# Optimization experiments

Measured on AMD Instinct MI355X. Metric: run time of the kernel, lower is better.

Reference implementation:

```python
import jax, jax.numpy as jnp
import numpy as np

B, N, RIN, ROUT, DEMB, FIN, FE, E, ITERS = 64, 128, 32, 64, 64, 64, 16, 65536, 3
NTOT = B * N


def gnn(x, edge_index, edge_feat, Ws, Wm, We, b):
    # edge-conditioned message passing: [NTOT, Fin] -> [NTOT, Fout]
    src, dst = edge_index[0], edge_index[1]
    msg = jax.nn.relu(x[src] @ Wm + edge_feat @ We)          # [E, Fout]
    agg = jax.ops.segment_sum(msg, dst, num_segments=x.shape[0])
    return jax.nn.relu(x @ Ws + agg + b)


def setup_inputs() -> dict:
    key = jax.random.key(0)
    ks = jax.random.split(key, 20)
    s = 0.1
    return {
        "x_r": jax.random.normal(ks[0], (NTOT, FIN), jnp.float32),
        "edge_index_r": jax.random.randint(ks[1], (2, E), 0, NTOT),
        "edge_feat_r": jax.random.normal(ks[2], (E, FE), jnp.float32),
        "x_p": jax.random.normal(ks[3], (NTOT, FIN), jnp.float32),
        "edge_index_p": jax.random.randint(ks[4], (2, E), 0, NTOT),
        "edge_feat_p": jax.random.normal(ks[5], (E, FE), jnp.float32),
        "r_mask": jnp.ones((B, N), dtype=bool),
        "p_mask": jnp.ones((B, N), dtype=bool),
        # gnn_1 params (FIN -> DEMB)
        "g1_Ws": jax.random.normal(ks[6], (FIN, DEMB)) * s,
        "g1_Wm": jax.random.normal(ks[7], (FIN, DEMB)) * s,
        "g1_We": jax.random.normal(ks[8], (FE, DEMB)) * s,
        "g1_b": jnp.zeros((DEMB,), jnp.float32),
        # gnn_2 params (RIN -> ROUT)
        "g2_Ws": jax.random.normal(ks[9], (RIN, ROUT)) * s,
        "g2_Wm": jax.random.normal(ks[10], (RIN, ROUT)) * s,
        "g2_We": jax.random.normal(ks[11], (FE, ROUT)) * s,
        "g2_b": jnp.zeros((ROUT,), jnp.float32),
        # consensus mlp (ROUT -> ROUT -> 1)
        "mlp_W1": jax.random.normal(ks[12], (ROUT, ROUT)) * s,
        "mlp_b1": jnp.zeros((ROUT,), jnp.float32),
        "mlp_W2": jax.random.normal(ks[13], (ROUT, 1)) * s,
        "mlp_b2": jnp.zeros((1,), jnp.float32),
    }


def reference(x_r, edge_index_r, edge_feat_r, x_p, edge_index_p, edge_feat_p,
              r_mask, p_mask,
              g1_Ws, g1_Wm, g1_We, g1_b,
              g2_Ws, g2_Wm, g2_We, g2_b,
              mlp_W1, mlp_b1, mlp_W2, mlp_b2):
    # node embeddings via gnn_1, then dense-batch to [B, N, DEMB]
    h_r = gnn(x_r, edge_index_r, edge_feat_r, g1_Ws, g1_Wm, g1_We, g1_b).reshape(B, N, DEMB)
    h_p = gnn(x_p, edge_index_p, edge_feat_p, g1_Ws, g1_Wm, g1_We, g1_b).reshape(B, N, DEMB)

    M_hat = jnp.einsum('brd,bpd->brp', h_r, h_p)             # [B, N_r, N_p]
    M_mask = r_mask[:, :, None] & p_mask[:, None, :]
    M_0 = jax.nn.softmax(M_hat, axis=-1).reshape(NTOT, N)    # packed (full mask)

    rkey = jax.random.key(42)
    for it in range(ITERS):
        M = jax.nn.softmax(M_hat, axis=-1)
        rf_r = jax.random.normal(jax.random.fold_in(rkey, it), (B, N, RIN), jnp.float32)
        rf_p = jnp.einsum('brp,bri->bpi', M, rf_r)           # M^T @ rand
        o_r = gnn(rf_r.reshape(NTOT, RIN), edge_index_r, edge_feat_r,
                  g2_Ws, g2_Wm, g2_We, g2_b).reshape(B, N, ROUT)
        o_p = gnn(rf_p.reshape(NTOT, RIN), edge_index_p, edge_feat_p,
                  g2_Ws, g2_Wm, g2_We, g2_b).reshape(B, N, ROUT)
        D = o_r[:, :, None, :] - o_p[:, None, :, :]          # [B, N_r, N_p, ROUT]
        upd = (jax.nn.relu(D @ mlp_W1 + mlp_b1) @ mlp_W2 + mlp_b2)[..., 0]
        M_hat = M_hat + jnp.where(M_mask, upd, 0.0)

    M_T = jax.nn.softmax(M_hat, axis=-1).reshape(NTOT, N)
    return (M_0, M_T)
```

## Files before the change

### kernel.cpp

```cpp
#include <hip/hip_runtime.h>

constexpr int kE = 65536, kNTOT = 8192;

__host__ __device__ __forceinline__ void tf_round(unsigned& x0, unsigned& x1, int r) {
  x0 += x1;
  x1 = (x1 << r) | (x1 >> (32 - r));
  x1 ^= x0;
}
__host__ __device__ __forceinline__ void tf2x32(unsigned k0, unsigned k1,
                                                unsigned& x0, unsigned& x1) {
  unsigned ks2 = k0 ^ k1 ^ 0x1BD11BDAu;
  x0 += k0; x1 += k1;
  tf_round(x0,x1,13); tf_round(x0,x1,15); tf_round(x0,x1,26); tf_round(x0,x1,6);
  x0 += k1; x1 += ks2 + 1u;
  tf_round(x0,x1,17); tf_round(x0,x1,29); tf_round(x0,x1,16); tf_round(x0,x1,24);
  x0 += ks2; x1 += k0 + 2u;
  tf_round(x0,x1,13); tf_round(x0,x1,15); tf_round(x0,x1,26); tf_round(x0,x1,6);
  x0 += k0; x1 += k1 + 3u;
  tf_round(x0,x1,17); tf_round(x0,x1,29); tf_round(x0,x1,16); tf_round(x0,x1,24);
  x0 += k1; x1 += ks2 + 4u;
  tf_round(x0,x1,13); tf_round(x0,x1,15); tf_round(x0,x1,26); tf_round(x0,x1,6);
  x0 += ks2; x1 += k0 + 5u;
}

__device__ __forceinline__ float bits_to_normal(unsigned bits) {
  float f = __uint_as_float((bits >> 9) | 0x3f800000u) - 1.0f;
  const float LO = -0.99999994f;
  float u = fmaf(f, 2.0f, LO);
  u = fmaxf(u, LO);
  float w = -log1pf(-u * u);
  float p;
  if (w < 5.0f) {
    w -= 2.5f;
    p = 2.81022636e-08f;
    p = fmaf(p, w, 3.43273939e-07f);
    p = fmaf(p, w, -3.5233877e-06f);
    p = fmaf(p, w, -4.39150654e-06f);
    p = fmaf(p, w, 0.00021858087f);
    p = fmaf(p, w, -0.00125372503f);
    p = fmaf(p, w, -0.00417768164f);
    p = fmaf(p, w, 0.246640727f);
    p = fmaf(p, w, 1.50140941f);
  } else {
    w = sqrtf(w) - 3.0f;
    p = -0.000200214257f;
    p = fmaf(p, w, 0.000100950558f);
    p = fmaf(p, w, 0.00134934322f);
    p = fmaf(p, w, -0.00367342844f);
    p = fmaf(p, w, 0.00573950773f);
    p = fmaf(p, w, -0.0076224613f);
    p = fmaf(p, w, 0.00943887047f);
    p = fmaf(p, w, 1.00167406f);
    p = fmaf(p, w, 2.83297682f);
  }
  return 1.41421356f * (p * u);
}

__device__ __forceinline__ float redmax32(float v) {
#pragma unroll
  for (int o = 16; o > 0; o >>= 1) v = fmaxf(v, __shfl_xor(v, o));
  return v;
}
__device__ __forceinline__ float redsum32(float v) {
#pragma unroll
  for (int o = 16; o > 0; o >>= 1) v += __shfl_xor(v, o);
  return v;
}

__global__ __launch_bounds__(256) void hist_kern(const int* __restrict__ eiR,
                                                 const int* __restrict__ eiP,
                                                 int* __restrict__ offR,
                                                 int* __restrict__ offP,
                                                 float* __restrict__ aggz,
                                                 float* __restrict__ rfpz) {
  int i = blockIdx.x * 256 + threadIdx.x;
  float4 z4 = make_float4(0.f, 0.f, 0.f, 0.f);
  float4* z = reinterpret_cast<float4*>(aggz) + i * 2;
  z[0] = z4; z[1] = z4;
  reinterpret_cast<float2*>(rfpz)[i] = make_float2(0.f, 0.f);
  const int* ei = (i < kE) ? eiR : eiP;
  int* off = (i < kE) ? offR : offP;
  int e = i & (kE - 1);
  atomicAdd(&off[ei[kE + e]], 1);
}

__global__ __launch_bounds__(256) void scan_kern(int* __restrict__ offR,
                                                 int* __restrict__ offP) {
  int* off = blockIdx.x ? offP : offR;
  int t = threadIdx.x;
  int base = t * 32;
  int v[32];
#pragma unroll
  for (int i = 0; i < 32; ++i) v[i] = off[base + i];
  int sum = 0;
#pragma unroll
  for (int i = 0; i < 32; ++i) sum += v[i];
  int lane = t & 63, w = t >> 6;
  int incl = sum;
#pragma unroll
  for (int o = 1; o < 64; o <<= 1) {
    int y = __shfl_up(incl, o);
    if (lane >= o) incl += y;
  }
  __shared__ int wsum[4];
  if (lane == 63) wsum[w] = incl;
  __syncthreads();
  int woff = 0;
#pragma unroll
  for (int i = 0; i < 4; ++i) if (i < w) woff += wsum[i];
  int running = woff + incl - sum;
#pragma unroll
  for (int i = 0; i < 32; ++i) {
    off[base + i] = running;
    running += v[i];
  }
}

__global__ __launch_bounds__(256) void scatter_kern(
    const int* __restrict__ eiR, const int* __restrict__ eiP,
    int* __restrict__ offR, int* __restrict__ offP,
    int* __restrict__ permR, int* __restrict__ permP,
    int* __restrict__ srcsR, int* __restrict__ srcsP,
    int* __restrict__ dstsR, int* __restrict__ dstsP) {
  int i = blockIdx.x * 256 + threadIdx.x;
  const int* ei = (i < kE) ? eiR : eiP;
  int* off = (i < kE) ? offR : offP;
  int* perm = (i < kE) ? permR : permP;
  int* srcs = (i < kE) ? srcsR : srcsP;
  int* dsts = (i < kE) ? dstsR : dstsP;
  int e = i & (kE - 1);
  int dst = ei[kE + e];
  int pos = atomicAdd(&off[dst], 1);
  perm[pos] = e;
  srcs[pos] = ei[e];
  dsts[pos] = dst;
}

template <int KK>
__global__ __launch_bounds__(256) void xw_gemm(
    const float* __restrict__ inR, const float* __restrict__ inP,
    float* __restrict__ xwR, float* __restrict__ xwP,
    const float* __restrict__ W) {
  __shared__ float sX[KK][68];
  __shared__ float sW[KK][68];
  bool isP = blockIdx.x >= 128;
  const float* in = isP ? inP : inR;
  float* xw = isP ? xwP : xwR;
  int n0 = (blockIdx.x & 127) * 64;
  int t = threadIdx.x;
#pragma unroll
  for (int idx = 0; idx < KK * 64 / 1024; ++idx) {
    int q = t * 4 + idx * 1024;
    int k = q >> 6, j = q & 63;
    *reinterpret_cast<float4*>(&sW[k][j]) = *reinterpret_cast<const float4*>(W + q);
    int r = q / KK, kk = q & (KK - 1);
    float4 v = *reinterpret_cast<const float4*>(in + (size_t)n0 * KK + q);
    sX[kk][r] = v.x; sX[kk + 1][r] = v.y; sX[kk + 2][r] = v.z; sX[kk + 3][r] = v.w;
  }
  __syncthreads();
  int tn = (t & 15) * 4, tj = (t >> 4) * 4;
  float acc[4][4] = {};
#pragma unroll 8
  for (int k = 0; k < KK; ++k) {
    float4 a = *reinterpret_cast<const float4*>(&sX[k][tn]);
    float4 b = *reinterpret_cast<const float4*>(&sW[k][tj]);
    acc[0][0] = fmaf(a.x, b.x, acc[0][0]); acc[0][1] = fmaf(a.x, b.y, acc[0][1]);
    acc[0][2] = fmaf(a.x, b.z, acc[0][2]); acc[0][3] = fmaf(a.x, b.w, acc[0][3]);
    acc[1][0] = fmaf(a.y, b.x, acc[1][0]); acc[1][1] = fmaf(a.y, b.y, acc[1][1]);
    acc[1][2] = fmaf(a.y, b.z, acc[1][2]); acc[1][3] = fmaf(a.y, b.w, acc[1][3]);
    acc[2][0] = fmaf(a.z, b.x, acc[2][0]); acc[2][1] = fmaf(a.z, b.y, acc[2][1]);
    acc[2][2] = fmaf(a.z, b.z, acc[2][2]); acc[2][3] = fmaf(a.z, b.w, acc[2][3]);
    acc[3][0] = fmaf(a.w, b.x, acc[3][0]); acc[3][1] = fmaf(a.w, b.y, acc[3][1]);
    acc[3][2] = fmaf(a.w, b.z, acc[3][2]); acc[3][3] = fmaf(a.w, b.w, acc[3][3]);
  }
#pragma unroll
  for (int i = 0; i < 4; ++i) {
    *reinterpret_cast<float4*>(&xw[(size_t)(n0 + tn + i) * 64 + tj]) =
        make_float4(acc[i][0], acc[i][1], acc[i][2], acc[i][3]);
  }
}

__global__ __launch_bounds__(256) void msg_edge(
    const float* __restrict__ xwR, const float* __restrict__ efR,
    const int* __restrict__ srcsR, const int* __restrict__ permR,
    const int* __restrict__ dstsR, float* __restrict__ aggR,
    const float* __restrict__ xwP, const float* __restrict__ efP,
    const int* __restrict__ srcsP, const int* __restrict__ permP,
    const int* __restrict__ dstsP, float* __restrict__ aggP,
    const float* __restrict__ We) {
  __shared__ float sEF[16][68];
  __shared__ float sW[16][68];
  __shared__ float sOut[64][68];
  __shared__ int sDst[64];
  __shared__ int sSrc[64];
  __shared__ int sPerm[64];
  bool isP = blockIdx.x >= 1024;
  const float* xw = isP ? xwP : xwR;
  const float* ef = isP ? efP : efR;
  const int* srcs = isP ? srcsP : srcsR;
  const int* perm = isP ? permP : permR;
  const int* dsts = isP ? dstsP : dstsR;
  float* agg = isP ? aggP : aggR;
  int i0 = (blockIdx.x & 1023) * 64;
  int t = threadIdx.x;
  {
    int q = t * 4;
    int k = q >> 6, j = q & 63;
    *reinterpret_cast<float4*>(&sW[k][j]) = *reinterpret_cast<const float4*>(We + q);
  }
  if (t < 64) {
    sDst[t] = dsts[i0 + t];
    sSrc[t] = srcs[i0 + t];
    sPerm[t] = perm[i0 + t];
  }
  __syncthreads();
  {
    int l = t & 3;
    int g = t >> 2;
    int rb = g >> 2;
    int kq = g & 3;
    int gbase = (t & 63) & ~3;
    int k4 = kq * 4;
    int r = rb * 4 + l;
    const float* rptr = ef + (size_t)sPerm[r] * 16 + k4;
    float4 v = *reinterpret_cast<const float4*>(rptr);
    float vc[4] = {v.x, v.y, v.z, v.w};
    float out[4];
#pragma unroll
    for (int c = 0; c < 4; ++c) {
      float val = vc[(l - c) & 3];
      out[(l + c) & 3] = __shfl(val, gbase + ((l + c) & 3), 64);
    }
    *reinterpret_cast<float4*>(&sEF[k4 + l][rb * 4]) =
        make_float4(out[0], out[1], out[2], out[3]);
  }
  __syncthreads();
  int tn = (t & 15) * 4, tj = (t >> 4) * 4;
  float acc[4][4] = {};
#pragma unroll
  for (int k = 0; k < 16; ++k) {
    float4 a = *reinterpret_cast<const float4*>(&sEF[k][tn]);
    float4 b = *reinterpret_cast<const float4*>(&sW[k][tj]);
    acc[0][0] = fmaf(a.x, b.x, acc[0][0]); acc[0][1] = fmaf(a.x, b.y, acc[0][1]);
    acc[0][2] = fmaf(a.x, b.z, acc[0][2]); acc[0][3] = fmaf(a.x, b.w, acc[0][3]);
    acc[1][0] = fmaf(a.y, b.x, acc[1][0]); acc[1][1] = fmaf(a.y, b.y, acc[1][1]);
    acc[1][2] = fmaf(a.y, b.z, acc[1][2]); acc[1][3] = fmaf(a.y, b.w, acc[1][3]);
    acc[2][0] = fmaf(a.z, b.x, acc[2][0]); acc[2][1] = fmaf(a.z, b.y, acc[2][1]);
    acc[2][2] = fmaf(a.z, b.z, acc[2][2]); acc[2][3] = fmaf(a.z, b.w, acc[2][3]);
    acc[3][0] = fmaf(a.w, b.x, acc[3][0]); acc[3][1] = fmaf(a.w, b.y, acc[3][1]);
    acc[3][2] = fmaf(a.w, b.z, acc[3][2]); acc[3][3] = fmaf(a.w, b.w, acc[3][3]);
  }
#pragma unroll
  for (int i = 0; i < 4; ++i) {
    float4 g = *reinterpret_cast<const float4*>(xw + (size_t)sSrc[tn + i] * 64 + tj);
    *reinterpret_cast<float4*>(&sOut[tn + i][tj]) =
        make_float4(fmaxf(acc[i][0] + g.x, 0.f), fmaxf(acc[i][1] + g.y, 0.f),
                    fmaxf(acc[i][2] + g.z, 0.f), fmaxf(acc[i][3] + g.w, 0.f));
  }
  __syncthreads();
  int col = t & 63;
  int r0l = (t >> 6) * 16;
  float run = 0.f;
  int rd = sDst[r0l];
#pragma unroll
  for (int r = 0; r < 16; ++r) {
    int d = sDst[r0l + r];
    if (d != rd) {
      unsafeAtomicAdd(&agg[(size_t)rd * 64 + col], run);
      run = 0.f; rd = d;
    }
    run += sOut[r0l + r][col];
  }
  unsafeAtomicAdd(&agg[(size_t)rd * 64 + col], run);
}

__global__ __launch_bounds__(256) void node1_gemm(
    const float* __restrict__ xR, float* __restrict__ aggR, float* __restrict__ hR,
    const float* __restrict__ xP, float* __restrict__ aggP, float* __restrict__ hP,
    const float* __restrict__ Ws, const float* __restrict__ bias) {
  __shared__ float sX[64][68];
  __shared__ float sW[64][68];
  bool isP = blockIdx.x >= 128;
  const float* x = isP ? xP : xR;
  float* agg = isP ? aggP : aggR;
  float* h = isP ? hP : hR;
  int n0 = (blockIdx.x & 127) * 64;
  int t = threadIdx.x;
#pragma unroll
  for (int idx = 0; idx < 4; ++idx) {
    int q = t * 4 + idx * 1024;
    int k = q >> 6, j = q & 63;
    *reinterpret_cast<float4*>(&sW[k][j]) = *reinterpret_cast<const float4*>(Ws + q);
    float4 v = *reinterpret_cast<const float4*>(x + (size_t)n0 * 64 + q);
    sX[j + 0][k] = v.x; sX[j + 1][k] = v.y; sX[j + 2][k] = v.z; sX[j + 3][k] = v.w;
  }
  __syncthreads();
  int tn = (t & 15) * 4, tj = (t >> 4) * 4;
  float acc[4][4] = {};
#pragma unroll 8
  for (int k = 0; k < 64; ++k) {
    float4 a = *reinterpret_cast<const float4*>(&sX[k][tn]);
    float4 b = *reinterpret_cast<const float4*>(&sW[k][tj]);
    acc[0][0] = fmaf(a.x, b.x, acc[0][0]); acc[0][1] = fmaf(a.x, b.y, acc[0][1]);
    acc[0][2] = fmaf(a.x, b.z, acc[0][2]); acc[0][3] = fmaf(a.x, b.w, acc[0][3]);
    acc[1][0] = fmaf(a.y, b.x, acc[1][0]); acc[1][1] = fmaf(a.y, b.y, acc[1][1]);
    acc[1][2] = fmaf(a.y, b.z, acc[1][2]); acc[1][3] = fmaf(a.y, b.w, acc[1][3]);
    acc[2][0] = fmaf(a.z, b.x, acc[2][0]); acc[2][1] = fmaf(a.z, b.y, acc[2][1]);
    acc[2][2] = fmaf(a.z, b.z, acc[2][2]); acc[2][3] = fmaf(a.z, b.w, acc[2][3]);
    acc[3][0] = fmaf(a.w, b.x, acc[3][0]); acc[3][1] = fmaf(a.w, b.y, acc[3][1]);
    acc[3][2] = fmaf(a.w, b.z, acc[3][2]); acc[3][3] = fmaf(a.w, b.w, acc[3][3]);
  }
  float4 bv = *reinterpret_cast<const float4*>(bias + tj);
  float4 z4 = make_float4(0.f, 0.f, 0.f, 0.f);
#pragma unroll
  for (int i = 0; i < 4; ++i) {
    int n = n0 + tn + i;
    float4 g = *reinterpret_cast<const float4*>(&agg[(size_t)n * 64 + tj]);
    *reinterpret_cast<float4*>(&agg[(size_t)n * 64 + tj]) = z4;
    float4 o;
    o.x = fmaxf(acc[i][0] + g.x + bv.x, 0.f);
    o.y = fmaxf(acc[i][1] + g.y + bv.y, 0.f);
    o.z = fmaxf(acc[i][2] + g.z + bv.z, 0.f);
    o.w = fmaxf(acc[i][3] + g.w + bv.w, 0.f);
    *reinterpret_cast<float4*>(&h[(size_t)n * 64 + tj]) = o;
  }
}

__device__ __forceinline__ void rfp_partial(const float sm[16][128],
                                            const float rfb[16][32],
                                            float* __restrict__ rfpB, int t) {
  float rfc[16];
  int iw = t & 31;
#pragma unroll
  for (int r = 0; r < 16; ++r) rfc[r] = rfb[r][iw];
#pragma unroll
  for (int rep = 0; rep < 16; ++rep) {
    int p = rep * 8 + (t >> 5);
    float a = 0.f;
#pragma unroll
    for (int r = 0; r < 16; ++r) a = fmaf(sm[r][p], rfc[r], a);
    unsafeAtomicAdd(&rfpB[p * 32 + iw], a);
  }
}

__device__ __forceinline__ void gen_rfr_tile(float* __restrict__ rfr,
                                             float rfb[16][32], int b, int r0,
                                             int t, unsigned fk0, unsigned fk1) {
  unsigned base = (unsigned)((b * 128 + r0) * 32);
#pragma unroll
  for (int q = 0; q < 2; ++q) {
    unsigned j = (unsigned)(q * 256 + t);
    unsigned i = base + j;
    unsigned a0 = 0u, a1 = i;
    tf2x32(fk0, fk1, a0, a1);
    float v = bits_to_normal(a0 ^ a1);
    rfr[i] = v;
    rfb[j >> 5][j & 31] = v;
  }
}

__global__ __launch_bounds__(256) void mhat_soft(
    const float* __restrict__ hR, const float* __restrict__ hP,
    float* __restrict__ Mhat, float* __restrict__ M0out,
    float* __restrict__ rfr, float* __restrict__ rfp,
    unsigned fk0, unsigned fk1) {
  __shared__ float hr[16][66];
  __shared__ float hp[128][66];
  __shared__ float sm[16][128];
  __shared__ float rfb[16][32];
  int gid = blockIdx.x, t = threadIdx.x;
  int b = gid >> 3, r0 = (gid & 7) * 16;
  gen_rfr_tile(rfr, rfb, b, r0, t, fk0, fk1);
  const float* hrG = hR + ((size_t)(b * 128 + r0)) * 64;
  {
    int q = t * 4; int r = q >> 6, d = q & 63;
    float4 v = *reinterpret_cast<const float4*>(hrG + q);
    hr[r][d] = v.x; hr[r][d + 1] = v.y; hr[r][d + 2] = v.z; hr[r][d + 3] = v.w;
  }
  const float* hpG = hP + (size_t)b * 128 * 64;
#pragma unroll
  for (int rep = 0; rep < 8; ++rep) {
    int q = (rep * 256 + t) * 4; int p = q >> 6, d = q & 63;
    float4 v = *reinterpret_cast<const float4*>(hpG + q);
    hp[p][d] = v.x; hp[p][d + 1] = v.y; hp[p][d + 2] = v.z; hp[p][d + 3] = v.w;
  }
  __syncthreads();
  int tx = t & 31, ty = t >> 5;
  float acc[2][4] = {};
  for (int d = 0; d < 64; ++d) {
    float a0 = hr[ty][d], a1 = hr[ty + 8][d];
    float q0 = hp[tx][d], q1 = hp[tx + 32][d], q2 = hp[tx + 64][d], q3 = hp[tx + 96][d];
    acc[0][0] = fmaf(a0, q0, acc[0][0]); acc[0][1] = fmaf(a0, q1, acc[0][1]);
    acc[0][2] = fmaf(a0, q2, acc[0][2]); acc[0][3] = fmaf(a0, q3, acc[0][3]);
    acc[1][0] = fmaf(a1, q0, acc[1][0]); acc[1][1] = fmaf(a1, q1, acc[1][1]);
    acc[1][2] = fmaf(a1, q2, acc[1][2]); acc[1][3] = fmaf(a1, q3, acc[1][3]);
  }
#pragma unroll
  for (int ii = 0; ii < 2; ++ii) {
    int r = r0 + ty + 8 * ii;
    float* mrow = Mhat + ((size_t)(b * 128 + r)) * 128;
    mrow[tx] = acc[ii][0]; mrow[tx + 32] = acc[ii][1];
    mrow[tx + 64] = acc[ii][2]; mrow[tx + 96] = acc[ii][3];
    float mx = redmax32(fmaxf(fmaxf(acc[ii][0], acc[ii][1]), fmaxf(acc[ii][2], acc[ii][3])));
    float e0 = __expf(acc[ii][0] - mx), e1 = __expf(acc[ii][1] - mx);
    float e2 = __expf(acc[ii][2] - mx), e3 = __expf(acc[ii][3] - mx);
    float inv = 1.0f / redsum32(e0 + e1 + e2 + e3);
    float* orow = M0out + ((size_t)(b * 128 + r)) * 128;
    orow[tx] = e0 * inv; orow[tx + 32] = e1 * inv;
    orow[tx + 64] = e2 * inv; orow[tx + 96] = e3 * inv;
    int rl = ty + 8 * ii;
    sm[rl][tx] = e0 * inv; sm[rl][tx + 32] = e1 * inv;
    sm[rl][tx + 64] = e2 * inv; sm[rl][tx + 96] = e3 * inv;
  }
  __syncthreads();
  rfp_partial(sm, rfb, rfp + (size_t)b * 4096, t);
}

__global__ __launch_bounds__(256) void node2u_gemm(
    const float* __restrict__ rfR, float* __restrict__ aggR, float* __restrict__ uR,
    const float* __restrict__ rfP, float* __restrict__ aggP, float* __restrict__ uP,
    const float* __restrict__ Ws2, const float* __restrict__ g2b,
    const float* __restrict__ W1, const float* __restrict__ b1,
    float* __restrict__ rfp_clear) {
  __shared__ float sRF[32][68];
  __shared__ float sW2[32][68];
  __shared__ float sW1[64][68];
  __shared__ float sO[64][68];
  bool isP = blockIdx.x >= 128;
  const float* rf = isP ? rfP : rfR;
  float* agg = isP ? aggP : aggR;
  float* u = isP ? uP : uR;
  int n0 = (blockIdx.x & 127) * 64;
  int t = threadIdx.x;
#pragma unroll
  for (int idx = 0; idx < 4; ++idx) {
    int q = t * 4 + idx * 1024;
    *reinterpret_cast<float4*>(&sW1[q >> 6][q & 63]) = *reinterpret_cast<const float4*>(W1 + q);
  }
#pragma unroll
  for (int idx = 0; idx < 2; ++idx) {
    int q = t * 4 + idx * 1024;
    *reinterpret_cast<float4*>(&sW2[q >> 6][q & 63]) = *reinterpret_cast<const float4*>(Ws2 + q);
    int r = q >> 5, kk = q & 31;
    float4 v = *reinterpret_cast<const float4*>(rf + (size_t)(n0 + r) * 32 + kk);
    sRF[kk][r] = v.x; sRF[kk + 1][r] = v.y; sRF[kk + 2][r] = v.z; sRF[kk + 3][r] = v.w;
  }
  __syncthreads();
  if (isP) {
    float4 z4 = make_float4(0.f, 0.f, 0.f, 0.f);
    float4* rz = reinterpret_cast<float4*>(rfp_clear + (size_t)n0 * 32);
    rz[t * 2] = z4; rz[t * 2 + 1] = z4;
  }
  int tn = (t & 15) * 4, tj = (t >> 4) * 4;
  float acc[4][4] = {};
#pragma unroll 8
  for (int k = 0; k < 32; ++k) {
    float4 a = *reinterpret_cast<const float4*>(&sRF[k][tn]);
    float4 b = *reinterpret_cast<const float4*>(&sW2[k][tj]);
    acc[0][0] = fmaf(a.x, b.x, acc[0][0]); acc[0][1] = fmaf(a.x, b.y, acc[0][1]);
    acc[0][2] = fmaf(a.x, b.z, acc[0][2]); acc[0][3] = fmaf(a.x, b.w, acc[0][3]);
    acc[1][0] = fmaf(a.y, b.x, acc[1][0]); acc[1][1] = fmaf(a.y, b.y, acc[1][1]);
    acc[1][2] = fmaf(a.y, b.z, acc[1][2]); acc[1][3] = fmaf(a.y, b.w, acc[1][3]);
    acc[2][0] = fmaf(a.z, b.x, acc[2][0]); acc[2][1] = fmaf(a.z, b.y, acc[2][1]);
    acc[2][2] = fmaf(a.z, b.z, acc[2][2]); acc[2][3] = fmaf(a.z, b.w, acc[2][3]);
    acc[3][0] = fmaf(a.w, b.x, acc[3][0]); acc[3][1] = fmaf(a.w, b.y, acc[3][1]);
    acc[3][2] = fmaf(a.w, b.z, acc[3][2]); acc[3][3] = fmaf(a.w, b.w, acc[3][3]);
  }
  float4 bg = *reinterpret_cast<const float4*>(g2b + tj);
  float4 z4 = make_float4(0.f, 0.f, 0.f, 0.f);
#pragma unroll
  for (int i = 0; i < 4; ++i) {
    int n = n0 + tn + i;
    float4 g = *reinterpret_cast<const float4*>(&agg[(size_t)n * 64 + tj]);
    *reinterpret_cast<float4*>(&agg[(size_t)n * 64 + tj]) = z4;
    sO[tj + 0][tn + i] = fmaxf(acc[i][0] + g.x + bg.x, 0.f);
    sO[tj + 1][tn + i] = fmaxf(acc[i][1] + g.y + bg.y, 0.f);
    sO[tj + 2][tn + i] = fmaxf(acc[i][2] + g.z + bg.z, 0.f);
    sO[tj + 3][tn + i] = fmaxf(acc[i][3] + g.w + bg.w, 0.f);
  }
  __syncthreads();
  float acc2[4][4] = {};
#pragma unroll 8
  for (int k = 0; k < 64; ++k) {
    float4 a = *reinterpret_cast<const float4*>(&sO[k][tn]);
    float4 b = *reinterpret_cast<const float4*>(&sW1[k][tj]);
    acc2[0][0] = fmaf(a.x, b.x, acc2[0][0]); acc2[0][1] = fmaf(a.x, b.y, acc2[0][1]);
    acc2[0][2] = fmaf(a.x, b.z, acc2[0][2]); acc2[0][3] = fmaf(a.x, b.w, acc2[0][3]);
    acc2[1][0] = fmaf(a.y, b.x, acc2[1][0]); acc2[1][1] = fmaf(a.y, b.y, acc2[1][1]);
    acc2[1][2] = fmaf(a.y, b.z, acc2[1][2]); acc2[1][3] = fmaf(a.y, b.w, acc2[1][3]);
    acc2[2][0] = fmaf(a.z, b.x, acc2[2][0]); acc2[2][1] = fmaf(a.z, b.y, acc2[2][1]);
    acc2[2][2] = fmaf(a.z, b.z, acc2[2][2]); acc2[2][3] = fmaf(a.z, b.w, acc2[2][3]);
    acc2[3][0] = fmaf(a.w, b.x, acc2[3][0]); acc2[3][1] = fmaf(a.w, b.y, acc2[3][1]);
    acc2[3][2] = fmaf(a.w, b.z, acc2[3][2]); acc2[3][3] = fmaf(a.w, b.w, acc2[3][3]);
  }
  float4 b1v = make_float4(0.f, 0.f, 0.f, 0.f);
  if (!isP) b1v = *reinterpret_cast<const float4*>(b1 + tj);
#pragma unroll
  for (int i = 0; i < 4; ++i) {
    int n = n0 + tn + i;
    float4 o;
    o.x = acc2[i][0] + b1v.x; o.y = acc2[i][1] + b1v.y;
    o.z = acc2[i][2] + b1v.z; o.w = acc2[i][3] + b1v.w;
    *reinterpret_cast<float4*>(&u[(size_t)n * 64 + tj]) = o;
  }
}

__global__ __launch_bounds__(256) void upd_soft(
    const float* __restrict__ uR, const float* __restrict__ uP,
    const float* __restrict__ W2, const float* __restrict__ b2p,
    float* __restrict__ Mhat, float* __restrict__ outLast, int last,
    float* __restrict__ rfr, float* __restrict__ rfp,
    unsigned fk0, unsigned fk1) {
  __shared__ float sur[16][66];
  __shared__ float sup[128][66];
  __shared__ float sw2[64];
  __shared__ float sm[16][128];
  __shared__ float rfb[16][32];
  int gid = blockIdx.x, t = threadIdx.x;
  int b = gid >> 3, r0 = (gid & 7) * 16;
  if (!last) gen_rfr_tile(rfr, rfb, b, r0, t, fk0, fk1);
  const float* urG = uR + ((size_t)(b * 128 + r0)) * 64;
  {
    int q = t * 4; int r = q >> 6, d = q & 63;
    float4 v = *reinterpret_cast<const float4*>(urG + q);
    sur[r][d] = v.x; sur[r][d + 1] = v.y; sur[r][d + 2] = v.z; sur[r][d + 3] = v.w;
  }
  const float* upG = uP + (size_t)b * 128 * 64;
#pragma unroll
  for (int rep = 0; rep < 8; ++rep) {
    int q = (rep * 256 + t) * 4; int p = q >> 6, d = q & 63;
    float4 v = *reinterpret_cast<const float4*>(upG + q);
    sup[p][d] = v.x; sup[p][d + 1] = v.y; sup[p][d + 2] = v.z; sup[p][d + 3] = v.w;
  }
  if (t < 64) sw2[t] = W2[t];
  __syncthreads();
  int tx = t & 31, ty = t >> 5;
  float acc[2][4] = {};
  for (int j = 0; j < 64; ++j) {
    float w2v = sw2[j];
    float a0 = sur[ty][j], a1 = sur[ty + 8][j];
    float q0 = sup[tx][j], q1 = sup[tx + 32][j], q2 = sup[tx + 64][j], q3 = sup[tx + 96][j];
    acc[0][0] = fmaf(fmaxf(a0 - q0, 0.f), w2v, acc[0][0]);
    acc[0][1] = fmaf(fmaxf(a0 - q1, 0.f), w2v, acc[0][1]);
    acc[0][2] = fmaf(fmaxf(a0 - q2, 0.f), w2v, acc[0][2]);
    acc[0][3] = fmaf(fmaxf(a0 - q3, 0.f), w2v, acc[0][3]);
    acc[1][0] = fmaf(fmaxf(a1 - q0, 0.f), w2v, acc[1][0]);
    acc[1][1] = fmaf(fmaxf(a1 - q1, 0.f), w2v, acc[1][1]);
    acc[1][2] = fmaf(fmaxf(a1 - q2, 0.f), w2v, acc[1][2]);
    acc[1][3] = fmaf(fmaxf(a1 - q3, 0.f), w2v, acc[1][3]);
  }
  float b2v = b2p[0];
#pragma unroll
  for (int ii = 0; ii < 2; ++ii) {
    int r = r0 + ty + 8 * ii;
    float* mrow = Mhat + ((size_t)(b * 128 + r)) * 128;
    float m0 = mrow[tx] + acc[ii][0] + b2v;
    float m1 = mrow[tx + 32] + acc[ii][1] + b2v;
    float m2 = mrow[tx + 64] + acc[ii][2] + b2v;
    float m3 = mrow[tx + 96] + acc[ii][3] + b2v;
    if (!last) {
      mrow[tx] = m0; mrow[tx + 32] = m1; mrow[tx + 64] = m2; mrow[tx + 96] = m3;
    }
    float mx = redmax32(fmaxf(fmaxf(m0, m1), fmaxf(m2, m3)));
    float e0 = __expf(m0 - mx), e1 = __expf(m1 - mx);
    float e2 = __expf(m2 - mx), e3 = __expf(m3 - mx);
    float inv = 1.0f / redsum32(e0 + e1 + e2 + e3);
    if (last) {
      float* orow = outLast + ((size_t)(b * 128 + r)) * 128;
      orow[tx] = e0 * inv; orow[tx + 32] = e1 * inv;
      orow[tx + 64] = e2 * inv; orow[tx + 96] = e3 * inv;
    } else {
      int rl = ty + 8 * ii;
      sm[rl][tx] = e0 * inv; sm[rl][tx + 32] = e1 * inv;
      sm[rl][tx + 64] = e2 * inv; sm[rl][tx + 96] = e3 * inv;
    }
  }
  if (!last) {
    __syncthreads();
    rfp_partial(sm, rfb, rfp + (size_t)b * 4096, t);
  }
}

extern "C" void kernel_launch(void* const* d_in, const int* in_sizes, int n_in,
                              void* d_out, int out_size, void* d_ws, size_t ws_size,
                              hipStream_t stream) {
  (void)in_sizes; (void)n_in; (void)out_size; (void)ws_size;
  const float* x_r  = (const float*)d_in[0];
  const int*   ei_r = (const int*)d_in[1];
  const float* ef_r = (const float*)d_in[2];
  const float* x_p  = (const float*)d_in[3];
  const int*   ei_p = (const int*)d_in[4];
  const float* ef_p = (const float*)d_in[5];
  const float* g1_Ws = (const float*)d_in[8];
  const float* g1_Wm = (const float*)d_in[9];
  const float* g1_We = (const float*)d_in[10];
  const float* g1_b  = (const float*)d_in[11];
  const float* g2_Ws = (const float*)d_in[12];
  const float* g2_Wm = (const float*)d_in[13];
  const float* g2_We = (const float*)d_in[14];
  const float* g2_b  = (const float*)d_in[15];
  const float* W1 = (const float*)d_in[16];
  const float* b1 = (const float*)d_in[17];
  const float* W2 = (const float*)d_in[18];
  const float* b2 = (const float*)d_in[19];
  float* out = (float*)d_out;

  float* ws = (float*)d_ws;
  float* h_r   = ws;
  float* h_p   = h_r + 524288;
  float* Mhat  = h_p + 524288;
  float* rfr   = Mhat + 1048576;
  float* rfp   = rfr + 262144;
  float* u_r   = rfp + 262144;
  float* u_p   = u_r + 524288;
  float* agg_r = u_p + 524288;
  float* agg_p = agg_r + 524288;
  float* xw_r  = agg_p + 524288;
  float* xw_p  = xw_r + 524288;
  int* ib      = (int*)(xw_p + 524288);
  int* off_r  = ib;
  int* off_p  = off_r + 8192;
  int* perm_r = off_p + 8192;
  int* perm_p = perm_r + 65536;
  int* srcs_r = perm_p + 65536;
  int* srcs_p = srcs_r + 65536;
  int* dsts_r = srcs_p + 65536;
  int* dsts_p = dsts_r + 65536;

  unsigned fk0[3], fk1[3];
  for (int it = 0; it < 3; ++it) {
    unsigned a = 0u, c = (unsigned)it;
    tf2x32(0u, 42u, a, c);
    fk0[it] = a; fk1[it] = c;
  }

  hipMemsetAsync(off_r, 0, 2 * 8192 * sizeof(int), stream);
  hist_kern<<<512, 256, 0, stream>>>(ei_r, ei_p, off_r, off_p, agg_r, rfp);
  scan_kern<<<2, 256, 0, stream>>>(off_r, off_p);
  scatter_kern<<<512, 256, 0, stream>>>(ei_r, ei_p, off_r, off_p,
                                        perm_r, perm_p, srcs_r, srcs_p,
                                        dsts_r, dsts_p);

  xw_gemm<64><<<256, 256, 0, stream>>>(x_r, x_p, xw_r, xw_p, g1_Wm);
  msg_edge<<<2048, 256, 0, stream>>>(xw_r, ef_r, srcs_r, perm_r, dsts_r, agg_r,
                                     xw_p, ef_p, srcs_p, perm_p, dsts_p, agg_p,
                                     g1_We);
  node1_gemm<<<256, 256, 0, stream>>>(x_r, agg_r, h_r, x_p, agg_p, h_p, g1_Ws, g1_b);
  mhat_soft<<<512, 256, 0, stream>>>(h_r, h_p, Mhat, out, rfr, rfp, fk0[0], fk1[0]);

  for (int it = 0; it < 3; ++it) {
    xw_gemm<32><<<256, 256, 0, stream>>>(rfr, rfp, xw_r, xw_p, g2_Wm);
    msg_edge<<<2048, 256, 0, stream>>>(xw_r, ef_r, srcs_r, perm_r, dsts_r, agg_r,
                                       xw_p, ef_p, srcs_p, perm_p, dsts_p, agg_p,
                                       g2_We);
    node2u_gemm<<<256, 256, 0, stream>>>(rfr, agg_r, u_r, rfp, agg_p, u_p,
                                         g2_Ws, g2_b, W1, b1, rfp);
    int last = (it == 2);
    upd_soft<<<512, 256, 0, stream>>>(u_r, u_p, W2, b2, Mhat,
                                      out + 1048576, last,
                                      rfr, rfp,
                                      fk0[it < 2 ? it + 1 : 0], fk1[it < 2 ? it + 1 : 0]);
  }
}
```

Baseline: 284.2 us.

## Precompute loop-invariant edge-feature projection and fuse rf_r projection into softmax kernels

The edge_feat @ g2_We product does not change across iterations, so it is now computed once inside the first message kernel and stored per edge (two 16 MB buffers). The per-iteration message kernel then only gathers that stored projection plus the source projection, with no edge-feature GEMM and no permuted edge-feature loads. The rf_r @ Wm projection is computed inside the kernels that generate rf_r, which leaves a smaller GEMM for rf_p only. The cost is extra workspace and global-memory traffic for reading 64-wide per-edge projections in place of 16-wide edge features, plus more shared memory in the softmax kernels.

Measured after the change: 289.8 us. Within noise of the previous version (+2.0%).

```diff
diff --git a/kernel.cpp b/kernel.cpp
--- a/kernel.cpp
+++ b/kernel.cpp
@@ -180,16 +180,55 @@
   }
 }
 
-__global__ __launch_bounds__(256) void msg_edge(
+__global__ __launch_bounds__(256) void xwp_gemm(
+    const float* __restrict__ rfp, float* __restrict__ xwP,
+    const float* __restrict__ W) {
+  __shared__ float sX[32][68];
+  __shared__ float sW[32][68];
+  int n0 = blockIdx.x * 64;
+  int t = threadIdx.x;
+#pragma unroll
+  for (int idx = 0; idx < 2; ++idx) {
+    int q = t * 4 + idx * 1024;
+    *reinterpret_cast<float4*>(&sW[q >> 6][q & 63]) = *reinterpret_cast<const float4*>(W + q);
+    int r = q >> 5, kk = q & 31;
+    float4 v = *reinterpret_cast<const float4*>(rfp + (size_t)n0 * 32 + q);
+    sX[kk][r] = v.x; sX[kk + 1][r] = v.y; sX[kk + 2][r] = v.z; sX[kk + 3][r] = v.w;
+  }
+  __syncthreads();
+  int tn = (t & 15) * 4, tj = (t >> 4) * 4;
+  float acc[4][4] = {};
+#pragma unroll 8
+  for (int k = 0; k < 32; ++k) {
+    float4 a = *reinterpret_cast<const float4*>(&sX[k][tn]);
+    float4 b = *reinterpret_cast<const float4*>(&sW[k][tj]);
+    acc[0][0] = fmaf(a.x, b.x, acc[0][0]); acc[0][1] = fmaf(a.x, b.y, acc[0][1]);
+    acc[0][2] = fmaf(a.x, b.z, acc[0][2]); acc[0][3] = fmaf(a.x, b.w, acc[0][3]);
+    acc[1][0] = fmaf(a.y, b.x, acc[1][0]); acc[1][1] = fmaf(a.y, b.y, acc[1][1]);
+    acc[1][2] = fmaf(a.y, b.z, acc[1][2]); acc[1][3] = fmaf(a.y, b.w, acc[1][3]);
+    acc[2][0] = fmaf(a.z, b.x, acc[2][0]); acc[2][1] = fmaf(a.z, b.y, acc[2][1]);
+    acc[2][2] = fmaf(a.z, b.z, acc[2][2]); acc[2][3] = fmaf(a.z, b.w, acc[2][3]);
+    acc[3][0] = fmaf(a.w, b.x, acc[3][0]); acc[3][1] = fmaf(a.w, b.y, acc[3][1]);
+    acc[3][2] = fmaf(a.w, b.z, acc[3][2]); acc[3][3] = fmaf(a.w, b.w, acc[3][3]);
+  }
+#pragma unroll
+  for (int i = 0; i < 4; ++i) {
+    *reinterpret_cast<float4*>(&xwP[(size_t)(n0 + tn + i) * 64 + tj]) =
+        make_float4(acc[i][0], acc[i][1], acc[i][2], acc[i][3]);
+  }
+}
+
+__global__ __launch_bounds__(256) void msg_edge_g1(
     const float* __restrict__ xwR, const float* __restrict__ efR,
     const int* __restrict__ srcsR, const int* __restrict__ permR,
-    const int* __restrict__ dstsR, float* __restrict__ aggR,
+    const int* __restrict__ dstsR, float* __restrict__ aggR, float* __restrict__ ew2R,
     const float* __restrict__ xwP, const float* __restrict__ efP,
     const int* __restrict__ srcsP, const int* __restrict__ permP,
-    const int* __restrict__ dstsP, float* __restrict__ aggP,
-    const float* __restrict__ We) {
+    const int* __restrict__ dstsP, float* __restrict__ aggP, float* __restrict__ ew2P,
+    const float* __restrict__ We1, const float* __restrict__ We2) {
   __shared__ float sEF[16][68];
-  __shared__ float sW[16][68];
+  __shared__ float sW1[16][68];
+  __shared__ float sW2[16][68];
   __shared__ float sOut[64][68];
   __shared__ int sDst[64];
   __shared__ int sSrc[64];
@@ -201,12 +240,14 @@
   const int* perm = isP ? permP : permR;
   const int* dsts = isP ? dstsP : dstsR;
   float* agg = isP ? aggP : aggR;
+  float* ew2 = isP ? ew2P : ew2R;
   int i0 = (blockIdx.x & 1023) * 64;
   int t = threadIdx.x;
   {
     int q = t * 4;
     int k = q >> 6, j = q & 63;
-    *reinterpret_cast<float4*>(&sW[k][j]) = *reinterpret_cast<const float4*>(We + q);
+    *reinterpret_cast<float4*>(&sW1[k][j]) = *reinterpret_cast<const float4*>(We1 + q);
+    *reinterpret_cast<float4*>(&sW2[k][j]) = *reinterpret_cast<const float4*>(We2 + q);
   }
   if (t < 64) {
     sDst[t] = dsts[i0 + t];
@@ -237,10 +278,12 @@
   __syncthreads();
   int tn = (t & 15) * 4, tj = (t >> 4) * 4;
   float acc[4][4] = {};
+  float ac2[4][4] = {};
 #pragma unroll
   for (int k = 0; k < 16; ++k) {
     float4 a = *reinterpret_cast<const float4*>(&sEF[k][tn]);
-    float4 b = *reinterpret_cast<const float4*>(&sW[k][tj]);
+    float4 b = *reinterpret_cast<const float4*>(&sW1[k][tj]);
+    float4 c = *reinterpret_cast<const float4*>(&sW2[k][tj]);
     acc[0][0] = fmaf(a.x, b.x, acc[0][0]); acc[0][1] = fmaf(a.x, b.y, acc[0][1]);
     acc[0][2] = fmaf(a.x, b.z, acc[0][2]); acc[0][3] = fmaf(a.x, b.w, acc[0][3]);
     acc[1][0] = fmaf(a.y, b.x, acc[1][0]); acc[1][1] = fmaf(a.y, b.y, acc[1][1]);
@@ -249,13 +292,72 @@
     acc[2][2] = fmaf(a.z, b.z, acc[2][2]); acc[2][3] = fmaf(a.z, b.w, acc[2][3]);
     acc[3][0] = fmaf(a.w, b.x, acc[3][0]); acc[3][1] = fmaf(a.w, b.y, acc[3][1]);
     acc[3][2] = fmaf(a.w, b.z, acc[3][2]); acc[3][3] = fmaf(a.w, b.w, acc[3][3]);
+    ac2[0][0] = fmaf(a.x, c.x, ac2[0][0]); ac2[0][1] = fmaf(a.x, c.y, ac2[0][1]);
+    ac2[0][2] = fmaf(a.x, c.z, ac2[0][2]); ac2[0][3] = fmaf(a.x, c.w, ac2[0][3]);
+    ac2[1][0] = fmaf(a.y, c.x, ac2[1][0]); ac2[1][1] = fmaf(a.y, c.y, ac2[1][1]);
+    ac2[1][2] = fmaf(a.y, c.z, ac2[1][2]); ac2[1][3] = fmaf(a.y, c.w, ac2[1][3]);
+    ac2[2][0] = fmaf(a.z, c.x, ac2[2][0]); ac2[2][1] = fmaf(a.z, c.y, ac2[2][1]);
+    ac2[2][2] = fmaf(a.z, c.z, ac2[2][2]); ac2[2][3] = fmaf(a.z, c.w, ac2[2][3]);
+    ac2[3][0] = fmaf(a.w, c.x, ac2[3][0]); ac2[3][1] = fmaf(a.w, c.y, ac2[3][1]);
+    ac2[3][2] = fmaf(a.w, c.z, ac2[3][2]); ac2[3][3] = fmaf(a.w, c.w, ac2[3][3]);
   }
 #pragma unroll
   for (int i = 0; i < 4; ++i) {
+    *reinterpret_cast<float4*>(&ew2[(size_t)(i0 + tn + i) * 64 + tj]) =
+        make_float4(ac2[i][0], ac2[i][1], ac2[i][2], ac2[i][3]);
     float4 g = *reinterpret_cast<const float4*>(xw + (size_t)sSrc[tn + i] * 64 + tj);
     *reinterpret_cast<float4*>(&sOut[tn + i][tj]) =
         make_float4(fmaxf(acc[i][0] + g.x, 0.f), fmaxf(acc[i][1] + g.y, 0.f),
                     fmaxf(acc[i][2] + g.z, 0.f), fmaxf(acc[i][3] + g.w, 0.f));
+  }
+  __syncthreads();
+  int col = t & 63;
+  int r0l = (t >> 6) * 16;
+  float run = 0.f;
+  int rd = sDst[r0l];
+#pragma unroll
+  for (int r = 0; r < 16; ++r) {
+    int d = sDst[r0l + r];
+    if (d != rd) {
+      unsafeAtomicAdd(&agg[(size_t)rd * 64 + col], run);
+      run = 0.f; rd = d;
+    }
+    run += sOut[r0l + r][col];
+  }
+  unsafeAtomicAdd(&agg[(size_t)rd * 64 + col], run);
+}
+
+__global__ __launch_bounds__(256) void msg_edge_it(
+    const float* __restrict__ xwR, const float* __restrict__ ew2R,
+    const int* __restrict__ srcsR, const int* __restrict__ dstsR,
+    float* __restrict__ aggR,
+    const float* __restrict__ xwP, const float* __restrict__ ew2P,
+    const int* __restrict__ srcsP, const int* __restrict__ dstsP,
+    float* __restrict__ aggP) {
+  __shared__ float sOut[64][68];
+  __shared__ int sDst[64];
+  __shared__ int sSrc[64];
+  bool isP = blockIdx.x >= 1024;
+  const float* xw = isP ? xwP : xwR;
+  const float* ew2 = isP ? ew2P : ew2R;
+  const int* srcs = isP ? srcsP : srcsR;
+  const int* dsts = isP ? dstsP : dstsR;
+  float* agg = isP ? aggP : aggR;
+  int i0 = (blockIdx.x & 1023) * 64;
+  int t = threadIdx.x;
+  if (t < 64) {
+    sDst[t] = dsts[i0 + t];
+    sSrc[t] = srcs[i0 + t];
+  }
+  __syncthreads();
+  int tn = (t & 15) * 4, tj = (t >> 4) * 4;
+#pragma unroll
+  for (int i = 0; i < 4; ++i) {
+    float4 e = *reinterpret_cast<const float4*>(ew2 + (size_t)(i0 + tn + i) * 64 + tj);
+    float4 g = *reinterpret_cast<const float4*>(xw + (size_t)sSrc[tn + i] * 64 + tj);
+    *reinterpret_cast<float4*>(&sOut[tn + i][tj]) =
+        make_float4(fmaxf(e.x + g.x, 0.f), fmaxf(e.y + g.y, 0.f),
+                    fmaxf(e.z + g.z, 0.f), fmaxf(e.w + g.w, 0.f));
   }
   __syncthreads();
   int col = t & 63;
@@ -359,15 +461,33 @@
   }
 }
 
+__device__ __forceinline__ void xwr_tile(const float rfb[16][32],
+                                         const float sWm2[32][68],
+                                         float* __restrict__ xwR,
+                                         int b, int r0, int t) {
+  int rl = t >> 4, c0 = (t & 15) * 4;
+  float4 a = make_float4(0.f, 0.f, 0.f, 0.f);
+#pragma unroll
+  for (int k = 0; k < 32; ++k) {
+    float rv = rfb[rl][k];
+    float4 w = *reinterpret_cast<const float4*>(&sWm2[k][c0]);
+    a.x = fmaf(rv, w.x, a.x); a.y = fmaf(rv, w.y, a.y);
+    a.z = fmaf(rv, w.z, a.z); a.w = fmaf(rv, w.w, a.w);
+  }
+  *reinterpret_cast<float4*>(&xwR[(size_t)(b * 128 + r0 + rl) * 64 + c0]) = a;
+}
+
 __global__ __launch_bounds__(256) void mhat_soft(
     const float* __restrict__ hR, const float* __restrict__ hP,
     float* __restrict__ Mhat, float* __restrict__ M0out,
-    float* __restrict__ rfr, float* __restrict__ rfp,
+    float* __restrict__ rfr, float* __restrict__ rfp, float* __restrict__ xwR,
+    const float* __restrict__ Wm2,
     unsigned fk0, unsigned fk1) {
   __shared__ float hr[16][66];
   __shared__ float hp[128][66];
   __shared__ float sm[16][128];
   __shared__ float rfb[16][32];
+  __shared__ float sWm2[32][68];
   int gid = blockIdx.x, t = threadIdx.x;
   int b = gid >> 3, r0 = (gid & 7) * 16;
   gen_rfr_tile(rfr, rfb, b, r0, t, fk0, fk1);
@@ -384,7 +504,14 @@
     float4 v = *reinterpret_cast<const float4*>(hpG + q);
     hp[p][d] = v.x; hp[p][d + 1] = v.y; hp[p][d + 2] = v.z; hp[p][d + 3] = v.w;
   }
-  __syncthreads();
+#pragma unroll
+  for (int idx = 0; idx < 2; ++idx) {
+    int q = t * 4 + idx * 1024;
+    *reinterpret_cast<float4*>(&sWm2[q >> 6][q & 63]) =
+        *reinterpret_cast<const float4*>(Wm2 + q);
+  }
+  __syncthreads();
+  xwr_tile(rfb, sWm2, xwR, b, r0, t);
   int tx = t & 31, ty = t >> 5;
   float acc[2][4] = {};
   for (int d = 0; d < 64; ++d) {
@@ -509,13 +636,15 @@
     const float* __restrict__ uR, const float* __restrict__ uP,
     const float* __restrict__ W2, const float* __restrict__ b2p,
     float* __restrict__ Mhat, float* __restrict__ outLast, int last,
-    float* __restrict__ rfr, float* __restrict__ rfp,
+    float* __restrict__ rfr, float* __restrict__ rfp, float* __restrict__ xwR,
+    const float* __restrict__ Wm2,
     unsigned fk0, unsigned fk1) {
   __shared__ float sur[16][66];
   __shared__ float sup[128][66];
   __shared__ float sw2[64];
   __shared__ float sm[16][128];
   __shared__ float rfb[16][32];
+  __shared__ float sWm2[32][68];
   int gid = blockIdx.x, t = threadIdx.x;
   int b = gid >> 3, r0 = (gid & 7) * 16;
   if (!last) gen_rfr_tile(rfr, rfb, b, r0, t, fk0, fk1);
@@ -533,7 +662,16 @@
     sup[p][d] = v.x; sup[p][d + 1] = v.y; sup[p][d + 2] = v.z; sup[p][d + 3] = v.w;
   }
   if (t < 64) sw2[t] = W2[t];
-  __syncthreads();
+  if (!last) {
+#pragma unroll
+    for (int idx = 0; idx < 2; ++idx) {
+      int q = t * 4 + idx * 1024;
+      *reinterpret_cast<float4*>(&sWm2[q >> 6][q & 63]) =
+          *reinterpret_cast<const float4*>(Wm2 + q);
+    }
+  }
+  __syncthreads();
+  if (!last) xwr_tile(rfb, sWm2, xwR, b, r0, t);
   int tx = t & 31, ty = t >> 5;
   float acc[2][4] = {};
   for (int j = 0; j < 64; ++j) {
@@ -617,7 +755,9 @@
   float* agg_p = agg_r + 524288;
   float* xw_r  = agg_p + 524288;
   float* xw_p  = xw_r + 524288;
-  int* ib      = (int*)(xw_p + 524288);
+  float* ew2_r = xw_p + 524288;
+  float* ew2_p = ew2_r + 4194304;
+  int* ib      = (int*)(ew2_p + 4194304);
   int* off_r  = ib;
   int* off_p  = off_r + 8192;
   int* perm_r = off_p + 8192;
@@ -642,23 +782,23 @@
                                         dsts_r, dsts_p);
 
   xw_gemm<64><<<256, 256, 0, stream>>>(x_r, x_p, xw_r, xw_p, g1_Wm);
-  msg_edge<<<2048, 256, 0, stream>>>(xw_r, ef_r, srcs_r, perm_r, dsts_r, agg_r,
-                                     xw_p, ef_p, srcs_p, perm_p, dsts_p, agg_p,
-                                     g1_We);
+  msg_edge_g1<<<2048, 256, 0, stream>>>(xw_r, ef_r, srcs_r, perm_r, dsts_r, agg_r, ew2_r,
+                                        xw_p, ef_p, srcs_p, perm_p, dsts_p, agg_p, ew2_p,
+                                        g1_We, g2_We);
   node1_gemm<<<256, 256, 0, stream>>>(x_r, agg_r, h_r, x_p, agg_p, h_p, g1_Ws, g1_b);
-  mhat_soft<<<512, 256, 0, stream>>>(h_r, h_p, Mhat, out, rfr, rfp, fk0[0], fk1[0]);
+  mhat_soft<<<512, 256, 0, stream>>>(h_r, h_p, Mhat, out, rfr, rfp, xw_r, g2_Wm,
+                                     fk0[0], fk1[0]);
 
   for (int it = 0; it < 3; ++it) {
-    xw_gemm<32><<<256, 256, 0, stream>>>(rfr, rfp, xw_r, xw_p, g2_Wm);
-    msg_edge<<<2048, 256, 0, stream>>>(xw_r, ef_r, srcs_r, perm_r, dsts_r, agg_r,
-                                       xw_p, ef_p, srcs_p, perm_p, dsts_p, agg_p,
-                                       g2_We);
+    xwp_gemm<<<128, 256, 0, stream>>>(rfp, xw_p, g2_Wm);
+    msg_edge_it<<<2048, 256, 0, stream>>>(xw_r, ew2_r, srcs_r, dsts_r, agg_r,
+                                          xw_p, ew2_p, srcs_p, dsts_p, agg_p);
     node2u_gemm<<<256, 256, 0, stream>>>(rfr, agg_r, u_r, rfp, agg_p, u_p,
                                          g2_Ws, g2_b, W1, b1, rfp);
     int last = (it == 2);
     upd_soft<<<512, 256, 0, stream>>>(u_r, u_p, W2, b2, Mhat,
                                       out + 1048576, last,
-                                      rfr, rfp,
+                                      rfr, rfp, xw_r, g2_Wm,
                                       fk0[it < 2 ? it + 1 : 0], fk1[it < 2 ? it + 1 : 0]);
   }
 }
```

## Fuse per-iteration message GEMM into softmax kernels via associativity

Applied to the files above, without the earlier changes.

Removes the separate xw_gemm launch inside each iteration. The softmax kernels now compute xw_r = rf_r @ Wm2 directly, and accumulate xw_p = M^T @ (rf_r @ Wm2) with atomics, using associativity in place of computing rf_p first. Zeroing of the xw_p accumulator moves into node1_gemm and node2u_gemm. This trades three kernel launches and their memory round-trips for roughly twice as many float atomics (64 columns instead of 32) and more shared memory per block, which may lower occupancy.

New measurement: 318.1 us. +11.9%, slower.

```diff
diff --git a/kernel.cpp b/kernel.cpp
--- a/kernel.cpp
+++ b/kernel.cpp
@@ -136,32 +136,30 @@
   dsts[pos] = dst;
 }
 
-template <int KK>
 __global__ __launch_bounds__(256) void xw_gemm(
     const float* __restrict__ inR, const float* __restrict__ inP,
     float* __restrict__ xwR, float* __restrict__ xwP,
     const float* __restrict__ W) {
-  __shared__ float sX[KK][68];
-  __shared__ float sW[KK][68];
+  __shared__ float sX[64][68];
+  __shared__ float sW[64][68];
   bool isP = blockIdx.x >= 128;
   const float* in = isP ? inP : inR;
   float* xw = isP ? xwP : xwR;
   int n0 = (blockIdx.x & 127) * 64;
   int t = threadIdx.x;
 #pragma unroll
-  for (int idx = 0; idx < KK * 64 / 1024; ++idx) {
+  for (int idx = 0; idx < 4; ++idx) {
     int q = t * 4 + idx * 1024;
     int k = q >> 6, j = q & 63;
     *reinterpret_cast<float4*>(&sW[k][j]) = *reinterpret_cast<const float4*>(W + q);
-    int r = q / KK, kk = q & (KK - 1);
-    float4 v = *reinterpret_cast<const float4*>(in + (size_t)n0 * KK + q);
-    sX[kk][r] = v.x; sX[kk + 1][r] = v.y; sX[kk + 2][r] = v.z; sX[kk + 3][r] = v.w;
+    float4 v = *reinterpret_cast<const float4*>(in + (size_t)n0 * 64 + q);
+    sX[j + 0][k] = v.x; sX[j + 1][k] = v.y; sX[j + 2][k] = v.z; sX[j + 3][k] = v.w;
   }
   __syncthreads();
   int tn = (t & 15) * 4, tj = (t >> 4) * 4;
   float acc[4][4] = {};
 #pragma unroll 8
-  for (int k = 0; k < KK; ++k) {
+  for (int k = 0; k < 64; ++k) {
     float4 a = *reinterpret_cast<const float4*>(&sX[k][tn]);
     float4 b = *reinterpret_cast<const float4*>(&sW[k][tj]);
     acc[0][0] = fmaf(a.x, b.x, acc[0][0]); acc[0][1] = fmaf(a.x, b.y, acc[0][1]);
@@ -277,7 +275,8 @@
 __global__ __launch_bounds__(256) void node1_gemm(
     const float* __restrict__ xR, float* __restrict__ aggR, float* __restrict__ hR,
     const float* __restrict__ xP, float* __restrict__ aggP, float* __restrict__ hP,
-    const float* __restrict__ Ws, const float* __restrict__ bias) {
+    const float* __restrict__ Ws, const float* __restrict__ bias,
+    float* __restrict__ xwp_clear) {
   __shared__ float sX[64][68];
   __shared__ float sW[64][68];
   bool isP = blockIdx.x >= 128;
@@ -286,6 +285,12 @@
   float* h = isP ? hP : hR;
   int n0 = (blockIdx.x & 127) * 64;
   int t = threadIdx.x;
+  if (isP) {
+    float4 z4 = make_float4(0.f, 0.f, 0.f, 0.f);
+    float4* xz = reinterpret_cast<float4*>(xwp_clear + (size_t)n0 * 64);
+#pragma unroll
+    for (int i = 0; i < 4; ++i) xz[t + i * 256] = z4;
+  }
 #pragma unroll
   for (int idx = 0; idx < 4; ++idx) {
     int q = t * 4 + idx * 1024;
@@ -343,6 +348,23 @@
   }
 }
 
+__device__ __forceinline__ void xwp_partial(const float sm[16][128],
+                                            const float xwt[16][68],
+                                            float* __restrict__ xwpB, int t) {
+  float xc[16];
+  int j = t & 63;
+#pragma unroll
+  for (int r = 0; r < 16; ++r) xc[r] = xwt[r][j];
+#pragma unroll
+  for (int rep = 0; rep < 32; ++rep) {
+    int p = rep * 4 + (t >> 6);
+    float a = 0.f;
+#pragma unroll
+    for (int r = 0; r < 16; ++r) a = fmaf(sm[r][p], xc[r], a);
+    unsafeAtomicAdd(&xwpB[(size_t)p * 64 + j], a);
+  }
+}
+
 __device__ __forceinline__ void gen_rfr_tile(float* __restrict__ rfr,
                                              float rfb[16][32], int b, int r0,
                                              int t, unsigned fk0, unsigned fk1) {
@@ -359,15 +381,37 @@
   }
 }
 
+__device__ __forceinline__ void xwr_tile(const float rfb[16][32],
+                                         const float sWm2[32][68],
+                                         float xwt[16][68],
+                                         float* __restrict__ xwR,
+                                         int b, int r0, int t) {
+  int rl = t >> 4, c0 = (t & 15) * 4;
+  float4 a = make_float4(0.f, 0.f, 0.f, 0.f);
+#pragma unroll
+  for (int k = 0; k < 32; ++k) {
+    float rv = rfb[rl][k];
+    float4 w = *reinterpret_cast<const float4*>(&sWm2[k][c0]);
+    a.x = fmaf(rv, w.x, a.x); a.y = fmaf(rv, w.y, a.y);
+    a.z = fmaf(rv, w.z, a.z); a.w = fmaf(rv, w.w, a.w);
+  }
+  *reinterpret_cast<float4*>(&xwt[rl][c0]) = a;
+  *reinterpret_cast<float4*>(&xwR[(size_t)(b * 128 + r0 + rl) * 64 + c0]) = a;
+}
+
 __global__ __launch_bounds__(256) void mhat_soft(
     const float* __restrict__ hR, const float* __restrict__ hP,
     float* __restrict__ Mhat, float* __restrict__ M0out,
     float* __restrict__ rfr, float* __restrict__ rfp,
+    float* __restrict__ xwR, float* __restrict__ xwP,
+    const float* __restrict__ Wm2,
     unsigned fk0, unsigned fk1) {
   __shared__ float hr[16][66];
   __shared__ float hp[128][66];
   __shared__ float sm[16][128];
   __shared__ float rfb[16][32];
+  __shared__ float sWm2[32][68];
+  __shared__ float xwt[16][68];
   int gid = blockIdx.x, t = threadIdx.x;
   int b = gid >> 3, r0 = (gid & 7) * 16;
   gen_rfr_tile(rfr, rfb, b, r0, t, fk0, fk1);
@@ -384,7 +428,14 @@
     float4 v = *reinterpret_cast<const float4*>(hpG + q);
     hp[p][d] = v.x; hp[p][d + 1] = v.y; hp[p][d + 2] = v.z; hp[p][d + 3] = v.w;
   }
-  __syncthreads();
+#pragma unroll
+  for (int idx = 0; idx < 2; ++idx) {
+    int q = t * 4 + idx * 1024;
+    *reinterpret_cast<float4*>(&sWm2[q >> 6][q & 63]) =
+        *reinterpret_cast<const float4*>(Wm2 + q);
+  }
+  __syncthreads();
+  xwr_tile(rfb, sWm2, xwt, xwR, b, r0, t);
   int tx = t & 31, ty = t >> 5;
   float acc[2][4] = {};
   for (int d = 0; d < 64; ++d) {
@@ -414,6 +465,7 @@
   }
   __syncthreads();
   rfp_partial(sm, rfb, rfp + (size_t)b * 4096, t);
+  xwp_partial(sm, xwt, xwP + (size_t)b * 8192, t);
 }
 
 __global__ __launch_bounds__(256) void node2u_gemm(
@@ -421,7 +473,7 @@
     const float* __restrict__ rfP, float* __restrict__ aggP, float* __restrict__ uP,
     const float* __restrict__ Ws2, const float* __restrict__ g2b,
     const float* __restrict__ W1, const float* __restrict__ b1,
-    float* __restrict__ rfp_clear) {
+    float* __restrict__ rfp_clear, float* __restrict__ xwp_clear) {
   __shared__ float sRF[32][68];
   __shared__ float sW2[32][68];
   __shared__ float sW1[64][68];
@@ -450,6 +502,9 @@
     float4 z4 = make_float4(0.f, 0.f, 0.f, 0.f);
     float4* rz = reinterpret_cast<float4*>(rfp_clear + (size_t)n0 * 32);
     rz[t * 2] = z4; rz[t * 2 + 1] = z4;
+    float4* xz = reinterpret_cast<float4*>(xwp_clear + (size_t)n0 * 64);
+#pragma unroll
+    for (int i = 0; i < 4; ++i) xz[t + i * 256] = z4;
   }
   int tn = (t & 15) * 4, tj = (t >> 4) * 4;
   float acc[4][4] = {};
@@ -510,12 +565,16 @@
     const float* __restrict__ W2, const float* __restrict__ b2p,
     float* __restrict__ Mhat, float* __restrict__ outLast, int last,
     float* __restrict__ rfr, float* __restrict__ rfp,
+    float* __restrict__ xwR, float* __restrict__ xwP,
+    const float* __restrict__ Wm2,
     unsigned fk0, unsigned fk1) {
   __shared__ float sur[16][66];
   __shared__ float sup[128][66];
   __shared__ float sw2[64];
   __shared__ float sm[16][128];
   __shared__ float rfb[16][32];
+  __shared__ float sWm2[32][68];
+  __shared__ float xwt[16][68];
   int gid = blockIdx.x, t = threadIdx.x;
   int b = gid >> 3, r0 = (gid & 7) * 16;
   if (!last) gen_rfr_tile(rfr, rfb, b, r0, t, fk0, fk1);
@@ -533,7 +592,16 @@
     sup[p][d] = v.x; sup[p][d + 1] = v.y; sup[p][d + 2] = v.z; sup[p][d + 3] = v.w;
   }
   if (t < 64) sw2[t] = W2[t];
-  __syncthreads();
+  if (!last) {
+#pragma unroll
+    for (int idx = 0; idx < 2; ++idx) {
+      int q = t * 4 + idx * 1024;
+      *reinterpret_cast<float4*>(&sWm2[q >> 6][q & 63]) =
+          *reinterpret_cast<const float4*>(Wm2 + q);
+    }
+  }
+  __syncthreads();
+  if (!last) xwr_tile(rfb, sWm2, xwt, xwR, b, r0, t);
   int tx = t & 31, ty = t >> 5;
   float acc[2][4] = {};
   for (int j = 0; j < 64; ++j) {
@@ -578,6 +646,7 @@
   if (!last) {
     __syncthreads();
     rfp_partial(sm, rfb, rfp + (size_t)b * 4096, t);
+    xwp_partial(sm, xwt, xwP + (size_t)b * 8192, t);
   }
 }
 
@@ -641,24 +710,25 @@
                                         perm_r, perm_p, srcs_r, srcs_p,
                                         dsts_r, dsts_p);
 
-  xw_gemm<64><<<256, 256, 0, stream>>>(x_r, x_p, xw_r, xw_p, g1_Wm);
+  xw_gemm<<<256, 256, 0, stream>>>(x_r, x_p, xw_r, xw_p, g1_Wm);
   msg_edge<<<2048, 256, 0, stream>>>(xw_r, ef_r, srcs_r, perm_r, dsts_r, agg_r,
                                      xw_p, ef_p, srcs_p, perm_p, dsts_p, agg_p,
                                      g1_We);
-  node1_gemm<<<256, 256, 0, stream>>>(x_r, agg_r, h_r, x_p, agg_p, h_p, g1_Ws, g1_b);
-  mhat_soft<<<512, 256, 0, stream>>>(h_r, h_p, Mhat, out, rfr, rfp, fk0[0], fk1[0]);
+  node1_gemm<<<256, 256, 0, stream>>>(x_r, agg_r, h_r, x_p, agg_p, h_p,
+                                      g1_Ws, g1_b, xw_p);
+  mhat_soft<<<512, 256, 0, stream>>>(h_r, h_p, Mhat, out, rfr, rfp, xw_r, xw_p,
+                                     g2_Wm, fk0[0], fk1[0]);
 
   for (int it = 0; it < 3; ++it) {
-    xw_gemm<32><<<256, 256, 0, stream>>>(rfr, rfp, xw_r, xw_p, g2_Wm);
     msg_edge<<<2048, 256, 0, stream>>>(xw_r, ef_r, srcs_r, perm_r, dsts_r, agg_r,
                                        xw_p, ef_p, srcs_p, perm_p, dsts_p, agg_p,
                                        g2_We);
     node2u_gemm<<<256, 256, 0, stream>>>(rfr, agg_r, u_r, rfp, agg_p, u_p,
-                                         g2_Ws, g2_b, W1, b1, rfp);
+                                         g2_Ws, g2_b, W1, b1, rfp, xw_p);
     int last = (it == 2);
     upd_soft<<<512, 256, 0, stream>>>(u_r, u_p, W2, b2, Mhat,
                                       out + 1048576, last,
-                                      rfr, rfp,
+                                      rfr, rfp, xw_r, xw_p, g2_Wm,
                                       fk0[it < 2 ? it + 1 : 0], fk1[it < 2 ? it + 1 : 0]);
   }
 }
```
